# Performance work log

Hardware: AMD Instinct MI355X
Metric: run time of the kernel (lower is better)

The kernel has to match this reference:

```python
import jax, jax.numpy as jnp
import numpy as np

N_NODES = 100000
N_EDGES = 1600000
N_GRAPHS = 128
D = 128          # input_dim == hidden_dim
OUT = 64         # output_dim (num classes)
L = 4            # num_layers - 1 GIN message-passing layers
BN_EPS = 1e-5


def setup_inputs() -> dict:
    key = jax.random.key(0)
    ks = jax.random.split(key, 12)
    s = 1.0 / np.sqrt(D)
    x = jax.random.normal(ks[0], (N_NODES, D), jnp.float32)
    edge_src = jax.random.randint(ks[1], (N_GRAPHS * 0 + N_EDGES,), 0, N_NODES, jnp.int32)
    edge_dst = jax.random.randint(ks[2], (N_EDGES,), 0, N_NODES, jnp.int32)
    graph_ids = jnp.sort(jax.random.randint(ks[3], (N_NODES,), 0, N_GRAPHS, jnp.int32))
    return {
        'x': x,
        'edge_src': edge_src,
        'edge_dst': edge_dst,
        'graph_ids': graph_ids,
        'eps': jnp.zeros((L,), jnp.float32),
        'W1': jax.random.normal(ks[4], (L, D, D), jnp.float32) * s,
        'b1': jnp.zeros((L, D), jnp.float32),
        'g1': jnp.ones((L, D), jnp.float32),
        'be1': jnp.zeros((L, D), jnp.float32),
        'W2': jax.random.normal(ks[5], (L, D, D), jnp.float32) * s,
        'b2': jnp.zeros((L, D), jnp.float32),
        'g2': jnp.ones((L, D), jnp.float32),
        'be2': jnp.zeros((L, D), jnp.float32),
        'predW': jax.random.normal(ks[6], (L + 1, D, OUT), jnp.float32) * s,
        'predb': jnp.zeros((L + 1, OUT), jnp.float32),
    }


def _bn(h, g, b):
    # BatchNorm1d in training mode: batch mean / biased variance over nodes
    mu = jnp.mean(h, axis=0)
    var = jnp.var(h, axis=0)
    return g * (h - mu) * jax.lax.rsqrt(var + BN_EPS) + b


def reference(x, edge_src, edge_dst, graph_ids, eps, W1, b1, g1, be1,
              W2, b2, g2, be2, predW, predb):
    n = x.shape[0]
    hidden = [x]
    h = x
    for l in range(L):
        # sparse Adj @ h : gather neighbor feats at edges, scatter-add to dst
        agg = jax.ops.segment_sum(h[edge_src], edge_dst, num_segments=n)
        pooled = agg + (1.0 + eps[l]) * h                      # GIN eps update
        z = jax.nn.relu(_bn(pooled @ W1[l] + b1[l], g1[l], be1[l]))  # MLP hidden
        z = z @ W2[l] + b2[l]                                  # MLP out
        h = jax.nn.relu(_bn(z, g2[l], be2[l]))                 # outer BN + relu
        hidden.append(h)
    # GIN readout: sum graph pooling + per-layer linear prediction (dropout p=0)
    score = jnp.zeros((N_GRAPHS, OUT), jnp.float32)
    for l, hl in enumerate(hidden):
        pooled_g = jax.ops.segment_sum(hl, graph_ids, num_segments=N_GRAPHS)
        score = score + pooled_g @ predW[l] + predb[l]
    return score
```

## Files before the change

kernel.cpp:

```cpp
#include <hip/hip_runtime.h>

#define NN 100000
#define NE 1600000
#define NG 128
#define DIM 128
#define OUTD 64
#define NL 4
#define SLCAP 48
#define RPB 256
#define RPBLKS ((NN + RPB - 1) / RPB)

typedef __attribute__((ext_vector_type(8))) short bf16x8;
typedef __attribute__((ext_vector_type(4))) float floatx4;
typedef __attribute__((ext_vector_type(2))) float floatx2;

__device__ __forceinline__ float bf_lo(unsigned u) {
    union { unsigned u; float f; } c; c.u = u << 16; return c.f;
}
__device__ __forceinline__ float bf_hi(unsigned u) {
    union { unsigned u; float f; } c; c.u = u & 0xffff0000u; return c.f;
}
__device__ __forceinline__ unsigned f2bf(float x) {
    union { float f; unsigned u; } c; c.f = x;
    return (c.u + 0x7fffu + ((c.u >> 16) & 1u)) >> 16;
}
__device__ __forceinline__ float bfs2f(short s) {
    union { unsigned u; float f; } c; c.u = ((unsigned)(unsigned short)s) << 16; return c.f;
}

__device__ __forceinline__ void bn_coef(const float* __restrict__ stat,
                                        const float* __restrict__ gamma,
                                        const float* __restrict__ beta,
                                        int f, float& a, float& c) {
    float mu = stat[f] * (1.0f / NN);
    float var = fmaf(-mu, mu, stat[DIM + f] * (1.0f / NN));
    a = gamma[f] * rsqrtf(var + 1e-5f);
    c = fmaf(-mu, a, beta[f]);
}

__global__ void build_links(const int* __restrict__ esrc, const int* __restrict__ edst,
                            int* __restrict__ head, int2* __restrict__ link) {
    int e = blockIdx.x * 256 + threadIdx.x;
    if (e < NE) {
        int d = edst[e];
        int prev = atomicExch(&head[d], e);
        link[e] = make_int2(prev, esrc[e]);
    }
}

__global__ __launch_bounds__(256)
void repack_slots(const int* __restrict__ head, const int2* __restrict__ link,
                  int* __restrict__ cnt, int* __restrict__ slot) {
    __shared__ int ls[SLCAP][RPB + 1];
    const int tid = threadIdx.x;
    const int n = blockIdx.x * RPB + tid;
    if (n < NN) {
        int e = head[n];
        int c = 0;
        while (e >= 0 && c < SLCAP) {
            int2 pr = link[e];
            ls[c][tid] = pr.y;
            e = pr.x;
            ++c;
        }
        cnt[n] = c;
    }
    __syncthreads();
    const int base = blockIdx.x * (RPB * SLCAP);
    for (int i = tid; i < RPB * SLCAP; i += 256) {
        int row = i / SLCAP, col = i - row * SLCAP;
        slot[base + i] = ls[col][row];
    }
}

__global__ void to_bf16(const float* __restrict__ x, unsigned* __restrict__ xb) {
    size_t i = ((size_t)blockIdx.x * 256 + threadIdx.x) * 4;
    float4 v = *(const float4*)(x + i);
    uint2 o;
    o.x = f2bf(v.x) | (f2bf(v.y) << 16);
    o.y = f2bf(v.z) | (f2bf(v.w) << 16);
    *(uint2*)(xb + i / 2) = o;
}

__global__ void build_wt(const float* __restrict__ W1, const float* __restrict__ W2,
                         unsigned short* __restrict__ Wt) {
    int b = blockIdx.x;
    const float* W = ((b & 1) ? W2 : W1) + (size_t)(b >> 1) * DIM * DIM;
    unsigned short* O = Wt + (size_t)b * DIM * DIM;
    int i = blockIdx.y * 2048 + threadIdx.x;
    for (int j = 0; j < 8; ++j, i += 256) {
        int k = i >> 7, n = i & 127;
        O[n * DIM + k] = (unsigned short)f2bf(W[i]);
    }
}

__global__ void csr_agg(const unsigned* __restrict__ hq, const int* __restrict__ cnt,
                        const int* __restrict__ slot, const float* __restrict__ eps, int l,
                        unsigned* __restrict__ outq) {
    const int t = threadIdx.x;
    const int node = blockIdx.x * 4 + (t >> 6);
    const int lane = t & 63;
    const int chunk = lane & 15;
    const int grp = lane >> 4;
    const uint4* __restrict__ h4 = (const uint4*)hq;

    const int deg = cnt[node];

    floatx2 acc[4];
    {
        uint4 sv = h4[(size_t)node * 16 + chunk];
        float e1 = (grp == 0) ? (1.0f + eps[l]) : 0.0f;
        const unsigned* p = (const unsigned*)&sv;
#pragma unroll
        for (int q = 0; q < 4; ++q) {
            floatx2 v; v.x = bf_lo(p[q]); v.y = bf_hi(p[q]);
            acc[q] = e1 * v;
        }
    }

    if (deg > 0) {
        const int iters = (deg + 15) >> 4;
        const int base = node * SLCAP;
        const int hi = base + deg - 1;
        const int j0 = base + grp;
        int idx[4];
#pragma unroll
        for (int q = 0; q < 4; ++q) {
            int j = j0 + q * 4;
            int v = slot[min(j, hi)];
            idx[q] = (j <= hi) ? v : NN;
        }

        for (int it = 0; it < iters; ++it) {
            uint4 u[4];
#pragma unroll
            for (int q = 0; q < 4; ++q) u[q] = h4[(size_t)idx[q] * 16 + chunk];

            if (it + 1 < iters) {
                const int jn = j0 + (it + 1) * 16;
#pragma unroll
                for (int q = 0; q < 4; ++q) {
                    int j = jn + q * 4;
                    int v = slot[min(j, hi)];
                    idx[q] = (j <= hi) ? v : NN;
                }
            }

#pragma unroll
            for (int q = 0; q < 4; ++q) {
                const unsigned* p = (const unsigned*)&u[q];
#pragma unroll
                for (int r = 0; r < 4; ++r) {
                    floatx2 v; v.x = bf_lo(p[r]); v.y = bf_hi(p[r]);
                    acc[r] += v;
                }
            }
        }
    }

#pragma unroll
    for (int r = 0; r < 4; ++r) {
        acc[r].x += __shfl_xor(acc[r].x, 16);
        acc[r].y += __shfl_xor(acc[r].y, 16);
        acc[r].x += __shfl_xor(acc[r].x, 32);
        acc[r].y += __shfl_xor(acc[r].y, 32);
    }
    if (grp == 0) {
        uint4 o;
        unsigned* po = (unsigned*)&o;
#pragma unroll
        for (int r = 0; r < 4; ++r)
            po[r] = f2bf(acc[r].x) | (f2bf(acc[r].y) << 16);
        ((uint4*)outq)[(size_t)node * 16 + chunk] = o;
    }
}

template<int TR>
__global__ __launch_bounds__(256, 2)
void gemm_mfma(const unsigned short* __restrict__ X, const unsigned short* __restrict__ Wt,
               const float* __restrict__ bias,
               const float* __restrict__ stat, const float* __restrict__ gamma,
               const float* __restrict__ beta,
               unsigned short* __restrict__ Y, float* __restrict__ ostat) {
    __shared__ unsigned short Ws[DIM * DIM];
    __shared__ float tatc[2 * DIM];
    float* red = (float*)Ws;
    const int t = threadIdx.x;
    const int w = t >> 6, lane = t & 63;
    const int quad = lane >> 4, m = lane & 15;
    const int rowbase = blockIdx.x * 128 + w * 32;

#pragma unroll
    for (int i = 0; i < 8; ++i) {
        int chunk = t + i * 256;
        int r = chunk >> 4, c = chunk & 15;
        ((uint4*)Ws)[(r << 4) | (c ^ (r & 15))] = ((const uint4*)Wt)[chunk];
    }
    if (TR && t < DIM) {
        float a, c;
        bn_coef(stat, gamma, beta, t, a, c);
        tatc[t] = a; tatc[DIM + t] = c;
    }

    bf16x8 a[2][4];
#pragma unroll
    for (int rt = 0; rt < 2; ++rt) {
        int row = rowbase + rt * 16 + m;
        if (row > NN - 1) row = NN - 1;
        const unsigned short* xr = X + (size_t)row * DIM + quad * 8;
#pragma unroll
        for (int ks = 0; ks < 4; ++ks)
            a[rt][ks] = *(const bf16x8*)(xr + ks * 32);
    }
    __syncthreads();
    if (TR) {
#pragma unroll
        for (int rt = 0; rt < 2; ++rt)
#pragma unroll
            for (int ks = 0; ks < 4; ++ks) {
                int kk = ks * 32 + quad * 8;
                bf16x8 v = a[rt][ks];
#pragma unroll
                for (int j = 0; j < 8; ++j) {
                    float fv = bfs2f(v[j]);
                    fv = fmaxf(fmaf(fv, tatc[kk + j], tatc[DIM + kk + j]), 0.f);
                    v[j] = (short)f2bf(fv);
                }
                a[rt][ks] = v;
            }
    }

    floatx4 acc[2][8];
#pragma unroll
    for (int rt = 0; rt < 2; ++rt)
#pragma unroll
        for (int ct = 0; ct < 8; ++ct) acc[rt][ct] = (floatx4)0.f;

#pragma unroll
    for (int ct = 0; ct < 8; ++ct) {
        const int row = ct * 16 + m;
        const bf16x8* wrow = (const bf16x8*)&Ws[row * DIM];
#pragma unroll
        for (int ks = 0; ks < 4; ++ks) {
            bf16x8 b = wrow[(ks * 4 + quad) ^ m];
            acc[0][ct] = __builtin_amdgcn_mfma_f32_16x16x32_bf16(a[0][ks], b, acc[0][ct], 0, 0, 0);
            acc[1][ct] = __builtin_amdgcn_mfma_f32_16x16x32_bf16(a[1][ks], b, acc[1][ct], 0, 0, 0);
        }
    }

    float sv[8], qv[8];
#pragma unroll
    for (int ct = 0; ct < 8; ++ct) {
        int col = ct * 16 + m;
        float bv = bias[col];
        float s = 0.f, q = 0.f;
#pragma unroll
        for (int rt = 0; rt < 2; ++rt) {
#pragma unroll
            for (int r = 0; r < 4; ++r) {
                int row = rowbase + rt * 16 + quad * 4 + r;
                float val = acc[rt][ct][r] + bv;
                if (row < NN) {
                    Y[(size_t)row * DIM + col] = (unsigned short)f2bf(val);
                    s += val;
                    q = fmaf(val, val, q);
                }
            }
        }
        s += __shfl_xor(s, 16); s += __shfl_xor(s, 32);
        q += __shfl_xor(q, 16); q += __shfl_xor(q, 32);
        sv[ct] = s; qv[ct] = q;
    }
    __syncthreads();
#pragma unroll
    for (int ct = 0; ct < 8; ++ct) {
        int col = ct * 16 + m;
        if (quad == 0) { red[w * 256 + col] = sv[ct]; red[w * 256 + 128 + col] = qv[ct]; }
    }
    __syncthreads();
    if (t < 256) {
        float tot = red[t] + red[256 + t] + red[512 + t] + red[768 + t];
        unsafeAtomicAdd(&ostat[t], tot);
    }
}

template<int TR>
__global__ void pool_nodes(const unsigned* __restrict__ hq, const int* __restrict__ gid,
                           const float* __restrict__ stat, const float* __restrict__ gamma,
                           const float* __restrict__ beta, float* __restrict__ pg) {
    const int lane = threadIdx.x;
    int start = blockIdx.x * 32;
    int end = start + 32;
    if (end > NN) end = NN;
    int f = lane * 2;
    float a0 = 0.f, c0 = 0.f, a1 = 0.f, c1 = 0.f;
    if (TR) {
        bn_coef(stat, gamma, beta, f, a0, c0);
        bn_coef(stat, gamma, beta, f + 1, a1, c1);
    }
    int cur = gid[start];
    float acc0 = 0.f, acc1 = 0.f;
    for (int i = start; i < end; ++i) {
        int g = gid[i];
        if (g != cur) {
            unsafeAtomicAdd(&pg[cur * DIM + f], acc0);
            unsafeAtomicAdd(&pg[cur * DIM + f + 1], acc1);
            acc0 = 0.f; acc1 = 0.f;
            cur = g;
        }
        unsigned u = hq[(size_t)i * 64 + lane];
        float x0 = bf_lo(u), x1 = bf_hi(u);
        if (TR) {
            x0 = fmaxf(fmaf(x0, a0, c0), 0.f);
            x1 = fmaxf(fmaf(x1, a1, c1), 0.f);
        }
        acc0 += x0; acc1 += x1;
    }
    unsafeAtomicAdd(&pg[cur * DIM + f], acc0);
    unsafeAtomicAdd(&pg[cur * DIM + f + 1], acc1);
}

template<int WRITE>
__global__ void norm_pool(const unsigned* __restrict__ hq, const int* __restrict__ gid,
                          const float* __restrict__ stat, const float* __restrict__ gamma,
                          const float* __restrict__ beta,
                          unsigned* __restrict__ outq, float* __restrict__ pg) {
    const int lane = threadIdx.x;
    int start = blockIdx.x * 32;
    int end = start + 32;
    if (end > NN) end = NN;
    int f = lane * 2;
    float a0, c0, a1, c1;
    bn_coef(stat, gamma, beta, f, a0, c0);
    bn_coef(stat, gamma, beta, f + 1, a1, c1);
    int cur = gid[start];
    float acc0 = 0.f, acc1 = 0.f;
    for (int i = start; i < end; ++i) {
        int g = gid[i];
        if (g != cur) {
            unsafeAtomicAdd(&pg[cur * DIM + f], acc0);
            unsafeAtomicAdd(&pg[cur * DIM + f + 1], acc1);
            acc0 = 0.f; acc1 = 0.f;
            cur = g;
        }
        unsigned u = hq[(size_t)i * 64 + lane];
        float x0 = fmaxf(fmaf(bf_lo(u), a0, c0), 0.f);
        float x1 = fmaxf(fmaf(bf_hi(u), a1, c1), 0.f);
        if (WRITE)
            outq[(size_t)i * 64 + lane] = f2bf(x0) | (f2bf(x1) << 16);
        acc0 += x0; acc1 += x1;
    }
    unsafeAtomicAdd(&pg[cur * DIM + f], acc0);
    unsafeAtomicAdd(&pg[cur * DIM + f + 1], acc1);
}

__global__ void final_score(const float* __restrict__ pg, const float* __restrict__ predW,
                            const float* __restrict__ predb, float* __restrict__ out) {
    int g = blockIdx.x;
    int o = threadIdx.x;
    float acc = 0.f;
    for (int l = 0; l <= NL; ++l) {
        acc += predb[l * OUTD + o];
        const float* pgr = pg + ((size_t)l * NG + g) * DIM;
        const float* w = predW + (size_t)l * DIM * OUTD;
#pragma unroll 8
        for (int k = 0; k < DIM; ++k)
            acc = fmaf(pgr[k], w[k * OUTD + o], acc);
    }
    out[g * OUTD + o] = acc;
}

extern "C" void kernel_launch(void* const* d_in, const int* in_sizes, int n_in,
                              void* d_out, int out_size, void* d_ws, size_t ws_size,
                              hipStream_t stream) {
    const float* x     = (const float*)d_in[0];
    const int*   esrc  = (const int*)d_in[1];
    const int*   edst  = (const int*)d_in[2];
    const int*   gid   = (const int*)d_in[3];
    const float* eps   = (const float*)d_in[4];
    const float* W1    = (const float*)d_in[5];
    const float* b1    = (const float*)d_in[6];
    const float* g1    = (const float*)d_in[7];
    const float* be1   = (const float*)d_in[8];
    const float* W2    = (const float*)d_in[9];
    const float* b2    = (const float*)d_in[10];
    const float* g2    = (const float*)d_in[11];
    const float* be2   = (const float*)d_in[12];
    const float* predW = (const float*)d_in[13];
    const float* predb = (const float*)d_in[14];
    float* out = (float*)d_out;

    unsigned short* XB = (unsigned short*)d_ws;
    unsigned short* A  = XB + (size_t)(NN + 1) * DIM;
    unsigned short* B  = A + (size_t)NN * DIM;
    unsigned short* WT = B + (size_t)NN * DIM;
    float* PG    = (float*)(WT + 8 * DIM * DIM);
    float* STATS = PG + 5 * NG * DIM;
    int* CNT  = (int*)(STATS + NL * 512);
    int* SLOT = CNT + NN;
    int*  HEAD = (int*)B;
    int2* LINK = (int2*)(HEAD + NN);

    hipMemsetAsync(PG, 0, (5 * NG * DIM + NL * 512) * sizeof(float), stream);
    hipMemsetAsync(XB + (size_t)NN * DIM, 0, DIM * sizeof(unsigned short), stream);
    hipMemsetAsync(HEAD, 0xFF, NN * sizeof(int), stream);

    build_links<<<(NE + 255) / 256, 256, 0, stream>>>(esrc, edst, HEAD, LINK);
    repack_slots<<<RPBLKS, 256, 0, stream>>>(HEAD, LINK, CNT, SLOT);
    to_bf16<<<(NN * DIM) / 1024, 256, 0, stream>>>(x, (unsigned*)XB);
    build_wt<<<dim3(8, 8), 256, 0, stream>>>(W1, W2, WT);

    const int poolBlocks = (NN + 31) / 32;
    const int aggBlocks  = (NN + 3) / 4;
    const int gemmBlocks = (NN + 127) / 128;

    for (int l = 0; l < NL; ++l) {
        float* STATL = STATS + l * 512;
        if (l == 0) {
            pool_nodes<0><<<poolBlocks, 64, 0, stream>>>((const unsigned*)XB, gid,
                                                         nullptr, nullptr, nullptr, PG);
        } else {
            const float* prevS = STATS + (l - 1) * 512 + 256;
            norm_pool<1><<<poolBlocks, 64, 0, stream>>>((const unsigned*)A, gid, prevS,
                                                        g2 + (l - 1) * DIM, be2 + (l - 1) * DIM,
                                                        (unsigned*)XB, PG + l * NG * DIM);
        }
        csr_agg<<<aggBlocks, 256, 0, stream>>>((const unsigned*)XB, CNT, SLOT, eps, l,
                                               (unsigned*)B);
        gemm_mfma<0><<<gemmBlocks, 256, 0, stream>>>(B, WT + (size_t)(2 * l) * DIM * DIM,
                                                     b1 + l * DIM, nullptr, nullptr, nullptr,
                                                     B, STATL);
        gemm_mfma<1><<<gemmBlocks, 256, 0, stream>>>(B, WT + (size_t)(2 * l + 1) * DIM * DIM,
                                                     b2 + l * DIM, STATL, g1 + l * DIM,
                                                     be1 + l * DIM, A, STATL + 256);
    }
    norm_pool<0><<<poolBlocks, 64, 0, stream>>>((const unsigned*)A, gid,
                                                STATS + (NL - 1) * 512 + 256,
                                                g2 + (NL - 1) * DIM, be2 + (NL - 1) * DIM,
                                                nullptr, PG + NL * NG * DIM);
    final_score<<<NG, OUTD, 0, stream>>>(PG, predW, predb, out);
}
```

Before: 846.0 us.

## Replace linked-list adjacency build with two-pass bucket sort by destination

Replaces the atomicExch linked-list construction and the serial pointer-chasing repack with a two-pass bucketing scheme. Edges are first counted per 256-node bucket in shared memory, then scattered into per-bucket arrays with packed (src, local dst) words. A second kernel groups each bucket's edges into per-node fixed-capacity slots in shared memory. This removes dependent random loads along the linked lists and global atomics per edge, at the cost of bounded bucket capacity (BCAP) and a larger shared-memory footprint.

```diff
diff --git a/kernel.cpp b/kernel.cpp
--- a/kernel.cpp
+++ b/kernel.cpp
@@ -7,8 +7,10 @@
 #define OUTD 64
 #define NL 4
 #define SLCAP 48
-#define RPB 256
-#define RPBLKS ((NN + RPB - 1) / RPB)
+#define NBKT 391
+#define BCAP 6144
+#define ECH 4096
+#define EBLKS ((NE + ECH - 1) / ECH)
 
 typedef __attribute__((ext_vector_type(8))) short bf16x8;
 typedef __attribute__((ext_vector_type(4))) float floatx4;
@@ -38,39 +40,53 @@
     c = fmaf(-mu, a, beta[f]);
 }
 
-__global__ void build_links(const int* __restrict__ esrc, const int* __restrict__ edst,
-                            int* __restrict__ head, int2* __restrict__ link) {
-    int e = blockIdx.x * 256 + threadIdx.x;
-    if (e < NE) {
-        int d = edst[e];
-        int prev = atomicExch(&head[d], e);
-        link[e] = make_int2(prev, esrc[e]);
-    }
-}
-
 __global__ __launch_bounds__(256)
-void repack_slots(const int* __restrict__ head, const int2* __restrict__ link,
-                  int* __restrict__ cnt, int* __restrict__ slot) {
-    __shared__ int ls[SLCAP][RPB + 1];
-    const int tid = threadIdx.x;
-    const int n = blockIdx.x * RPB + tid;
-    if (n < NN) {
-        int e = head[n];
-        int c = 0;
-        while (e >= 0 && c < SLCAP) {
-            int2 pr = link[e];
-            ls[c][tid] = pr.y;
-            e = pr.x;
-            ++c;
-        }
-        cnt[n] = c;
-    }
-    __syncthreads();
-    const int base = blockIdx.x * (RPB * SLCAP);
-    for (int i = tid; i < RPB * SLCAP; i += 256) {
-        int row = i / SLCAP, col = i - row * SLCAP;
-        slot[base + i] = ls[col][row];
-    }
+void bucketize(const int* __restrict__ esrc, const int* __restrict__ edst,
+               int* __restrict__ gcnt, unsigned* __restrict__ bkt) {
+    __shared__ int lh[NBKT];
+    for (int b = threadIdx.x; b < NBKT; b += 256) lh[b] = 0;
+    __syncthreads();
+    const int e0 = blockIdx.x * ECH;
+    const int e1 = min(e0 + ECH, NE);
+    for (int e = e0 + threadIdx.x; e < e1; e += 256)
+        atomicAdd(&lh[(unsigned)edst[e] >> 8], 1);
+    __syncthreads();
+    for (int b = threadIdx.x; b < NBKT; b += 256) {
+        int c = lh[b];
+        lh[b] = (c > 0) ? atomicAdd(&gcnt[b], c) : 0;
+    }
+    __syncthreads();
+    for (int e = e0 + threadIdx.x; e < e1; e += 256) {
+        unsigned d = (unsigned)edst[e];
+        unsigned b = d >> 8;
+        int p = atomicAdd(&lh[b], 1);
+        if (p < BCAP)
+            bkt[(size_t)b * BCAP + p] = (unsigned)esrc[e] | ((d & 255u) << 24);
+    }
+}
+
+__global__ __launch_bounds__(256)
+void bucket_to_slots(const unsigned* __restrict__ bkt, const int* __restrict__ gcnt,
+                     int* __restrict__ cnt, int* __restrict__ slot) {
+    __shared__ int lslot[256 * SLCAP];
+    __shared__ int lc[256];
+    const int b = blockIdx.x, t = threadIdx.x;
+    lc[t] = 0;
+    __syncthreads();
+    int ne = gcnt[b]; if (ne > BCAP) ne = BCAP;
+    const unsigned* be = bkt + (size_t)b * BCAP;
+    for (int i = t; i < ne; i += 256) {
+        unsigned v = be[i];
+        int local = v >> 24;
+        int pos = atomicAdd(&lc[local], 1);
+        if (pos < SLCAP) lslot[local * SLCAP + pos] = (int)(v & 0xFFFFFFu);
+    }
+    __syncthreads();
+    const int node = b * 256 + t;
+    if (node < NN) cnt[node] = min(lc[t], SLCAP);
+    const size_t base = (size_t)b * (256 * SLCAP);
+    for (int i = t; i < 256 * SLCAP; i += 256)
+        slot[base + i] = lslot[i];
 }
 
 __global__ void to_bf16(const float* __restrict__ x, unsigned* __restrict__ xb) {
@@ -396,17 +412,16 @@
     unsigned short* WT = B + (size_t)NN * DIM;
     float* PG    = (float*)(WT + 8 * DIM * DIM);
     float* STATS = PG + 5 * NG * DIM;
-    int* CNT  = (int*)(STATS + NL * 512);
+    int* GCNT = (int*)(STATS + NL * 512);
+    int* CNT  = GCNT + 512;
     int* SLOT = CNT + NN;
-    int*  HEAD = (int*)B;
-    int2* LINK = (int2*)(HEAD + NN);
-
-    hipMemsetAsync(PG, 0, (5 * NG * DIM + NL * 512) * sizeof(float), stream);
+    unsigned* BKT = (unsigned*)B;
+
+    hipMemsetAsync(PG, 0, (5 * NG * DIM + NL * 512 + 512) * sizeof(float), stream);
     hipMemsetAsync(XB + (size_t)NN * DIM, 0, DIM * sizeof(unsigned short), stream);
-    hipMemsetAsync(HEAD, 0xFF, NN * sizeof(int), stream);
-
-    build_links<<<(NE + 255) / 256, 256, 0, stream>>>(esrc, edst, HEAD, LINK);
-    repack_slots<<<RPBLKS, 256, 0, stream>>>(HEAD, LINK, CNT, SLOT);
+
+    bucketize<<<EBLKS, 256, 0, stream>>>(esrc, edst, GCNT, BKT);
+    bucket_to_slots<<<NBKT, 256, 0, stream>>>(BKT, GCNT, CNT, SLOT);
     to_bf16<<<(NN * DIM) / 1024, 256, 0, stream>>>(x, (unsigned*)XB);
     build_wt<<<dim3(8, 8), 256, 0, stream>>>(W1, W2, WT);
 
```

Result: faster. 795.4 us (-6.0%).
